# Optimization experiments

Measured on AMD Instinct MI355X. Metric: run time of the kernel, lower is better.

The kernel has to match this reference:

```python
import jax, jax.numpy as jnp
import numpy as np

N = 30000   # nodes
E = 600000  # edges (avg degree 20)
H = 128     # hidden_channels
L = 4       # num_layers
G = 64      # graphs in batch


def _init(key, shape, fan_in):
    return (jax.random.normal(key, shape, jnp.float32) / np.sqrt(fan_in)).astype(jnp.float32)


def setup_inputs() -> dict:
    key = jax.random.key(0)
    ks = jax.random.split(key, 24)
    x = jax.random.normal(ks[0], (N, 1), jnp.float32)
    pos = jax.random.normal(ks[1], (N, 3), jnp.float32)
    edge_index = jax.random.randint(ks[2], (2, E), 0, N, dtype=jnp.int32).astype(jnp.int64)
    batch = jnp.sort(jax.random.randint(ks[3], (N,), 0, G, dtype=jnp.int32)).astype(jnp.int64)

    emb_w = _init(ks[4], (1, H), 1)
    emb_b = jnp.zeros((H,), jnp.float32)

    # stacked per-layer params: msg MLP (2H+1 -> H -> H), node MLP (2H -> H -> H)
    msg_w1 = _init(ks[5], (L, 2 * H + 1, H), 2 * H + 1)
    msg_b1 = jnp.zeros((L, H), jnp.float32)
    msg_w2 = _init(ks[6], (L, H, H), H)
    msg_b2 = jnp.zeros((L, H), jnp.float32)
    node_w1 = _init(ks[7], (L, 2 * H, H), 2 * H)
    node_b1 = jnp.zeros((L, H), jnp.float32)
    node_w2 = _init(ks[8], (L, H, H), H)
    node_b2 = jnp.zeros((L, H), jnp.float32)

    out_w1 = _init(ks[9], (H, 32), H)
    out_b1 = jnp.zeros((32,), jnp.float32)
    out_w2 = _init(ks[10], (32, 1), 32)
    out_b2 = jnp.zeros((1,), jnp.float32)

    return {
        "x": x, "pos": pos, "edge_index": edge_index, "batch": batch,
        "emb_w": emb_w, "emb_b": emb_b,
        "msg_w1": msg_w1, "msg_b1": msg_b1, "msg_w2": msg_w2, "msg_b2": msg_b2,
        "node_w1": node_w1, "node_b1": node_b1, "node_w2": node_w2, "node_b2": node_b2,
        "out_w1": out_w1, "out_b1": out_b1, "out_w2": out_w2, "out_b2": out_b2,
    }


def reference(x, pos, edge_index, batch,
              emb_w, emb_b,
              msg_w1, msg_b1, msg_w2, msg_b2,
              node_w1, node_b1, node_w2, node_b2,
              out_w1, out_b1, out_w2, out_b2):
    row, col = edge_index[0], edge_index[1]  # row = source j, col = target i
    # edge scalar: squared distance (computed once, reused across layers)
    dist_sq = jnp.sum((pos[row] - pos[col]) ** 2, axis=-1, keepdims=True)  # [E,1]

    h = x @ emb_w + emb_b  # [N,H]
    for l in range(L):
        x_j = h[row]   # source features
        x_i = h[col]   # target features
        m = jnp.concatenate([x_i, x_j, dist_sq], axis=-1)           # [E, 2H+1]
        m = jax.nn.silu(m @ msg_w1[l] + msg_b1[l]) @ msg_w2[l] + msg_b2[l]  # [E,H]
        aggr = jax.ops.segment_sum(m, col, num_segments=N)          # scatter-add to targets
        nh = jnp.concatenate([h, aggr], axis=-1)                    # [N, 2H]
        h = jax.nn.silu(nh @ node_w1[l] + node_b1[l]) @ node_w2[l] + node_b2[l]
        # dropout omitted for deterministic reference (eval mode)

    g = jax.ops.segment_sum(h, batch, num_segments=G)               # global_add_pool [G,H]
    return jax.nn.silu(g @ out_w1 + out_b1) @ out_w2 + out_b2       # [G,1]
```

## Files before the change

### kernel.cpp

```cpp
#include <hip/hip_runtime.h>

typedef unsigned short u16;
typedef __bf16 bf16x8 __attribute__((ext_vector_type(8)));
typedef float f32x4 __attribute__((ext_vector_type(4)));

#define HN 128
#define TM 64
#define ASTRIDE 136
#define ECH 256

__device__ __forceinline__ u16 f2bf(float f) {
  union { float f; unsigned u; } v; v.f = f;
  unsigned r = v.u + 0x7fffu + ((v.u >> 16) & 1u);
  return (u16)(r >> 16);
}
__device__ __forceinline__ float bf2f(u16 v) {
  union { unsigned u; float f; } x; x.u = ((unsigned)v) << 16; return x.f;
}
__device__ __forceinline__ float bflo(unsigned v) {
  union { unsigned u; float f; } x; x.u = v << 16; return x.f;
}
__device__ __forceinline__ float bfhi(unsigned v) {
  union { unsigned u; float f; } x; x.u = v & 0xffff0000u; return x.f;
}
__device__ __forceinline__ float silu_f(float x) {
  float e = __builtin_amdgcn_exp2f(-1.442695041f * x);
  return x * __builtin_amdgcn_rcpf(1.f + e);
}

__global__ void pack_weights(const float* __restrict__ msg_w1, const float* __restrict__ msg_w2,
                             const float* __restrict__ node_w1, const float* __restrict__ node_w2,
                             u16* __restrict__ pw, int* __restrict__ deg,
                             float* __restrict__ g, int N_, int GH) {
  int id = blockIdx.x * 256 + threadIdx.x;
  if (id < N_) deg[id] = 0;
  if (id < GH) g[id] = 0.f;
  if (id >= 4 * 6 * 16384) return;
  int l = id / (6 * 16384);
  int rem = id % (6 * 16384);
  int m = rem / 16384;
  int e = rem % 16384;
  int kg = e >> 10;
  int n = (e >> 3) & 127;
  int j = e & 7;
  int k = kg * 8 + j;
  float v = 0.f;
  switch (m) {
    case 0: v = msg_w1[(l * 257 + k) * 128 + n]; break;
    case 1: v = msg_w1[(l * 257 + 128 + k) * 128 + n]; break;
    case 2: v = msg_w2[(l * 128 + k) * 128 + n]; break;
    case 3: v = node_w1[(l * 256 + k) * 128 + n]; break;
    case 4: v = node_w1[(l * 256 + 128 + k) * 128 + n]; break;
    case 5: v = node_w2[(l * 128 + k) * 128 + n]; break;
  }
  pw[id] = f2bf(v);
}

__device__ __forceinline__ void gemm64(const u16* s_A, const u16* s_W,
                                       int w, int quad, int m16, f32x4 acc[8]) {
#pragma unroll
  for (int ks = 0; ks < 4; ks++) {
    bf16x8 a = *(const bf16x8*)&s_A[(w * 16 + m16) * ASTRIDE + ks * 32 + quad * 8];
#pragma unroll
    for (int ct = 0; ct < 8; ct++) {
      bf16x8 b = *(const bf16x8*)&s_W[(ks * 4 + quad) * 1024 + (ct * 16 + m16) * 8];
      acc[ct] = __builtin_amdgcn_mfma_f32_16x16x32_bf16(a, b, acc[ct], 0, 0, 0);
    }
  }
}

__device__ __forceinline__ void gemm64_gb(const u16* s_A, const u16* __restrict__ gW,
                                          int w, int quad, int m16, f32x4 acc[8]) {
#pragma unroll
  for (int ks = 0; ks < 4; ks++) {
    bf16x8 a = *(const bf16x8*)&s_A[(w * 16 + m16) * ASTRIDE + ks * 32 + quad * 8];
#pragma unroll
    for (int ct = 0; ct < 8; ct++) {
      bf16x8 b = *(const bf16x8*)&gW[(ks * 4 + quad) * 1024 + (ct * 16 + m16) * 8];
      acc[ct] = __builtin_amdgcn_mfma_f32_16x16x32_bf16(a, b, acc[ct], 0, 0, 0);
    }
  }
}

__device__ __forceinline__ void gemm64_ra_gb(const bf16x8 aH[4], const u16* __restrict__ gW,
                                             int quad, int m16, f32x4 acc[8]) {
#pragma unroll
  for (int ks = 0; ks < 4; ks++) {
#pragma unroll
    for (int ct = 0; ct < 8; ct++) {
      bf16x8 b = *(const bf16x8*)&gW[(ks * 4 + quad) * 1024 + (ct * 16 + m16) * 8];
      acc[ct] = __builtin_amdgcn_mfma_f32_16x16x32_bf16(aH[ks], b, acc[ct], 0, 0, 0);
    }
  }
}

__global__ __launch_bounds__(256) void fold_kernel(
    const float* __restrict__ msg_w2, const float* __restrict__ node_w1,
    const float* __restrict__ msg_b2, const u16* __restrict__ pw,
    u16* __restrict__ pwc, float* __restrict__ vc) {
  __shared__ __align__(16) u16 s_A[TM * ASTRIDE];
  __shared__ __align__(16) u16 s_W[16384];
  const int t = threadIdx.x;
  const int w = t >> 6, lane = t & 63, quad = lane >> 4, m16 = lane & 15;
  const int b = blockIdx.x, l = b >> 1, half = b & 1;
  const int tile0 = half * 64;

  {
    int r = t >> 2, qo = (t & 3) * 32;
    const float4* src = (const float4*)(msg_w2 + (size_t)(l * 128 + tile0 + r) * 128 + qo);
    u16* dst = s_A + r * ASTRIDE + qo;
#pragma unroll
    for (int i = 0; i < 8; i++) {
      float4 v = src[i];
      ushort4 o;
      o.x = f2bf(v.x); o.y = f2bf(v.y); o.z = f2bf(v.z); o.w = f2bf(v.w);
      *(ushort4*)(dst + i * 4) = o;
    }
  }
  {
    const int4* src = (const int4*)(pw + (size_t)(l * 6 + 4) * 16384);
    int4* dst = (int4*)s_W;
#pragma unroll
    for (int i = 0; i < 8; i++) dst[t + i * 256] = src[t + i * 256];
  }
  __syncthreads();
  f32x4 acc[8];
#pragma unroll
  for (int ct = 0; ct < 8; ct++) acc[ct] = {0.f, 0.f, 0.f, 0.f};
  gemm64(s_A, s_W, w, quad, m16, acc);
#pragma unroll
  for (int ct = 0; ct < 8; ct++)
#pragma unroll
    for (int j = 0; j < 4; j++) {
      int k = tile0 + w * 16 + quad * 4 + j;
      int n = ct * 16 + m16;
      pwc[(size_t)l * 16384 + (k >> 3) * 1024 + n * 8 + (k & 7)] = f2bf(acc[ct][j]);
    }
  if (half == 0 && t < 128) {
    float s = 0.f;
    for (int np = 0; np < 128; np++)
      s += msg_b2[l * 128 + np] * node_w1[(size_t)(l * 256 + 128 + np) * 128 + t];
    vc[l * 128 + t] = s;
  }
}

__global__ void hist_kernel(const int* __restrict__ eidx, int* __restrict__ deg,
                            int* __restrict__ rnk, int E_) {
  int e = blockIdx.x * 256 + threadIdx.x;
  if (e < E_) rnk[e] = atomicAdd(&deg[eidx[E_ + e]], 1);
}

__global__ void scan1_kernel(const int* __restrict__ deg, int* __restrict__ off,
                             int* __restrict__ bsum, int n) {
  __shared__ int s[256];
  int t = threadIdx.x;
  int i = blockIdx.x * 256 + t;
  int v = (i < n) ? deg[i] : 0;
  s[t] = v;
  for (int d = 1; d < 256; d <<= 1) {
    __syncthreads();
    int x = (t >= d) ? s[t - d] : 0;
    __syncthreads();
    s[t] += x;
  }
  __syncthreads();
  if (i < n) off[i] = s[t] - v;
  if (t == 255) bsum[blockIdx.x] = s[255];
}

__global__ void scan2_kernel(int* __restrict__ bsum, int nb) {
  __shared__ int s[256];
  int t = threadIdx.x;
  int v = (t < nb) ? bsum[t] : 0;
  s[t] = v;
  for (int d = 1; d < 256; d <<= 1) {
    __syncthreads();
    int x = (t >= d) ? s[t - d] : 0;
    __syncthreads();
    s[t] += x;
  }
  __syncthreads();
  if (t < nb) bsum[t] = s[t] - v;
}

__global__ void scan3_kernel(int* __restrict__ off, const int* __restrict__ bsum, int n) {
  int i = blockIdx.x * 256 + threadIdx.x;
  if (i < n) off[i] += bsum[blockIdx.x];
}

__global__ void scatter_kernel(const int* __restrict__ eidx, const float* __restrict__ pos,
                               const int* __restrict__ off, const int* __restrict__ rnk,
                               int2* __restrict__ es8, int E_) {
  int e = blockIdx.x * 256 + threadIdx.x;
  if (e >= E_) return;
  int sr = eidx[e], tg = eidx[E_ + e];
  float dx = pos[sr * 3 + 0] - pos[tg * 3 + 0];
  float dy = pos[sr * 3 + 1] - pos[tg * 3 + 1];
  float dz = pos[sr * 3 + 2] - pos[tg * 3 + 2];
  float d = dx * dx + dy * dy + dz * dz;
  int p = off[tg] + rnk[e];
  int2 v;
  v.x = sr | (tg << 15);
  v.y = __float_as_int(d);
  es8[p] = v;
}

__global__ __launch_bounds__(256) void proj_kernel(
    const float* __restrict__ x, const float* __restrict__ emb_w,
    const float* __restrict__ emb_b, u16* __restrict__ hbf,
    u16* __restrict__ Pout, u16* __restrict__ Qout,
    const u16* __restrict__ pw, const float* __restrict__ b1,
    float* __restrict__ S, int NH4, int nblocks, int nnodes) {
  const int t = threadIdx.x;
  const int w = t >> 6, lane = t & 63, quad = lane >> 4, m16 = lane & 15;
  const int tile0 = blockIdx.x * TM;

  {
    float4* S4 = (float4*)S;
    int id = blockIdx.x * 256 + t;
    int stride = nblocks * 256;
    float4 z = {0.f, 0.f, 0.f, 0.f};
    for (int i = id; i < NH4; i += stride) S4[i] = z;
  }

  int nodem = tile0 + w * 16 + m16;
  bool live = nodem < nnodes;
  if (!live) nodem = nnodes - 1;
  float xv = x[nodem];
  bf16x8 aH[4];
#pragma unroll
  for (int ks = 0; ks < 4; ks++) {
    u16 hv[8];
#pragma unroll
    for (int i = 0; i < 8; i++) {
      int c = ks * 32 + quad * 8 + i;
      hv[i] = f2bf(xv * emb_w[c] + emb_b[c]);
    }
    aH[ks] = *(bf16x8*)hv;
    if (live) *(int4*)&hbf[(size_t)nodem * HN + ks * 32 + quad * 8] = *(int4*)hv;
  }
  float bb[8];
#pragma unroll
  for (int ct = 0; ct < 8; ct++) bb[ct] = b1[ct * 16 + m16];

  f32x4 acc[8];
#pragma unroll
  for (int ct = 0; ct < 8; ct++) acc[ct] = {0.f, 0.f, 0.f, 0.f};
  gemm64_ra_gb(aH, pw, quad, m16, acc);
#pragma unroll
  for (int ct = 0; ct < 8; ct++)
#pragma unroll
    for (int j = 0; j < 4; j++) {
      int n = tile0 + w * 16 + quad * 4 + j;
      if (n < nnodes) Pout[(size_t)n * HN + ct * 16 + m16] = f2bf(acc[ct][j] + bb[ct]);
    }
#pragma unroll
  for (int ct = 0; ct < 8; ct++) acc[ct] = {0.f, 0.f, 0.f, 0.f};
  gemm64_ra_gb(aH, pw + 16384, quad, m16, acc);
#pragma unroll
  for (int ct = 0; ct < 8; ct++)
#pragma unroll
    for (int j = 0; j < 4; j++) {
      int n = tile0 + w * 16 + quad * 4 + j;
      if (n < nnodes) Qout[(size_t)n * HN + ct * 16 + m16] = f2bf(acc[ct][j]);
    }
}

__device__ __forceinline__ void edge_step(
    int tg_s, float dd_s, unsigned qv,
    int& cur_s, float& p0, float& p1, float& s0, float& s1,
    const u16* __restrict__ P, float* __restrict__ S, int cp,
    float wd0, float wd1, int tprev_s, int tnext_s) {
  if (tg_s != cur_s) {
    if (cur_s >= 0) {
      float* dst = &S[(size_t)cur_s * HN + cp];
      if (cur_s == tprev_s || cur_s == tnext_s) {
        atomicAdd(dst, s0);
        atomicAdd(dst + 1, s1);
      } else {
        float2 v = {s0, s1};
        *(float2*)dst = v;
      }
    }
    cur_s = tg_s; s0 = 0.f; s1 = 0.f;
    int cg = tg_s < 0 ? 0 : tg_s;
    unsigned pv = *(const unsigned*)&P[(size_t)cg * HN + cp];
    p0 = bflo(pv); p1 = bfhi(pv);
  }
  float x0 = p0 + bflo(qv) + dd_s * wd0;
  float x1 = p1 + bfhi(qv) + dd_s * wd1;
  s0 += silu_f(x0);
  s1 += silu_f(x1);
}

__global__ __launch_bounds__(256) void edge_kernel(
    const u16* __restrict__ P, const u16* __restrict__ Q,
    float* __restrict__ S, const float* __restrict__ w1d,
    const int2* __restrict__ es8, int E_) {
  __shared__ int s_src[ECH + 8];
  __shared__ int s_tgt[ECH + 8];
  __shared__ float s_dist[ECH + 8];

  const int t = threadIdx.x;
  const int e0 = blockIdx.x * ECH;
  {
    int e = e0 + t;
    if (e < E_) {
      int2 v = es8[e];
      s_src[t] = v.x & 0x7fff;
      s_tgt[t] = v.x >> 15;
      s_dist[t] = __int_as_float(v.y);
    } else {
      s_src[t] = 0; s_tgt[t] = -1; s_dist[t] = 0.f;
    }
    if (t < 8) { s_src[ECH + t] = 0; s_tgt[ECH + t] = -1; s_dist[ECH + t] = 0.f; }
  }
  __syncthreads();

  const int lane = t & 63;
  const int w = t >> 6;
  const int cp = lane * 2;
  const int a = w * 64;
  const float2 wdv = *(const float2*)&w1d[cp];
  const float wd0 = wdv.x, wd1 = wdv.y;

  int tprev_s, tnext_s;
  if (w == 0) tprev_s = (e0 > 0) ? (es8[e0 - 1].x >> 15) : -2;
  else tprev_s = s_tgt[a - 1];
  if (w == 3) tnext_s = (e0 + ECH < E_) ? (es8[e0 + ECH].x >> 15) : -2;
  else tnext_s = s_tgt[a + 64];
  tprev_s = __builtin_amdgcn_readfirstlane(tprev_s);
  tnext_s = __builtin_amdgcn_readfirstlane(tnext_s);

  int tg[8];
  float dd[8];
  unsigned qv[8];
#pragma unroll
  for (int j = 0; j < 8; j++) {
    tg[j] = s_tgt[a + j];
    dd[j] = s_dist[a + j];
    qv[j] = *(const unsigned*)&Q[(size_t)s_src[a + j] * HN + cp];
  }

  int cur_s = -1;
  float s0 = 0.f, s1 = 0.f, p0 = 0.f, p1 = 0.f;

#pragma unroll
  for (int i = a; i < a + 64; i += 8) {
    int tgn[8];
    float ddn[8];
    unsigned qvn[8];
#pragma unroll
    for (int j = 0; j < 8; j++) {
      int idx = i + 8 + j;
      tgn[j] = s_tgt[idx];
      ddn[j] = s_dist[idx];
      qvn[j] = *(const unsigned*)&Q[(size_t)s_src[idx] * HN + cp];
    }
#pragma unroll
    for (int j = 0; j < 8; j++) {
      int tg_s = __builtin_amdgcn_readfirstlane(tg[j]);
      edge_step(tg_s, dd[j], qv[j], cur_s, p0, p1, s0, s1, P, S, cp, wd0, wd1, tprev_s, tnext_s);
    }
#pragma unroll
    for (int j = 0; j < 8; j++) { tg[j] = tgn[j]; dd[j] = ddn[j]; qv[j] = qvn[j]; }
  }

  if (cur_s >= 0) {
    float* dst = &S[(size_t)cur_s * HN + cp];
    if (cur_s == tprev_s || cur_s == tnext_s) {
      atomicAdd(dst, s0);
      atomicAdd(dst + 1, s1);
    } else {
      float2 v = {s0, s1};
      *(float2*)dst = v;
    }
  }
}

template <bool FUSE>
__global__ __launch_bounds__(256) void node_kernel(
    const u16* __restrict__ hbf, float* __restrict__ S, const int* __restrict__ deg,
    u16* __restrict__ hout, const u16* __restrict__ pwc, const float* __restrict__ vc,
    const u16* __restrict__ pwn, const float* __restrict__ b1, const float* __restrict__ b2,
    const u16* __restrict__ pw_next, const float* __restrict__ b1_next,
    u16* __restrict__ Pout, u16* __restrict__ Qout, int nnodes) {
  __shared__ __align__(16) u16 s_A[TM * ASTRIDE];
  const int t = threadIdx.x;
  const int w = t >> 6, lane = t & 63, quad = lane >> 4, m16 = lane & 15;
  const int tile0 = blockIdx.x * TM;
  const int rb = lane >> 2;
  const int qo = (lane & 3) * 32;
  u16* band = s_A + (w * 16) * ASTRIDE;

  int node_ = tile0 + w * 16 + rb;
  if (node_ >= nnodes) node_ = nnodes - 1;
  int nodem = tile0 + w * 16 + m16;
  if (nodem >= nnodes) nodem = nnodes - 1;

  float bb1[8], vcr[8], bb2[8], bbn[8];
#pragma unroll
  for (int ct = 0; ct < 8; ct++) {
    bb1[ct] = b1[ct * 16 + m16];
    vcr[ct] = vc[ct * 16 + m16];
    bb2[ct] = b2[ct * 16 + m16];
    bbn[ct] = FUSE ? b1_next[ct * 16 + m16] : 0.f;
  }

  {
    const float4* src = (const float4*)(S + (size_t)node_ * HN + qo);
    u16* dst = band + rb * ASTRIDE + qo;
#pragma unroll
    for (int i = 0; i < 8; i++) {
      float4 v = src[i];
      ushort4 o;
      o.x = f2bf(v.x); o.y = f2bf(v.y); o.z = f2bf(v.z); o.w = f2bf(v.w);
      *(ushort4*)(dst + i * 4) = o;
    }
    float4 z = {0.f, 0.f, 0.f, 0.f};
    float4* zd = (float4*)(S + (size_t)node_ * HN + qo);
#pragma unroll
    for (int i = 0; i < 8; i++) zd[i] = z;
  }
  asm volatile("s_waitcnt lgkmcnt(0)" ::: "memory");
  __builtin_amdgcn_sched_barrier(0);

  f32x4 acc[8];
#pragma unroll
  for (int ct = 0; ct < 8; ct++) acc[ct] = {0.f, 0.f, 0.f, 0.f};
  gemm64_gb(s_A, pwc, w, quad, m16, acc);

  bf16x8 aH[4];
#pragma unroll
  for (int ks = 0; ks < 4; ks++)
    aH[ks] = *(const bf16x8*)&hbf[(size_t)nodem * HN + ks * 32 + quad * 8];
  gemm64_ra_gb(aH, pwn, quad, m16, acc);

  {
    float degv[4];
#pragma unroll
    for (int j = 0; j < 4; j++) {
      int n = tile0 + w * 16 + quad * 4 + j;
      if (n >= nnodes) n = nnodes - 1;
      degv[j] = (float)deg[n];
    }
#pragma unroll
    for (int ct = 0; ct < 8; ct++)
#pragma unroll
      for (int j = 0; j < 4; j++) {
        int row = quad * 4 + j;
        float xv = acc[ct][j] + bb1[ct] + degv[j] * vcr[ct];
        band[row * ASTRIDE + ct * 16 + m16] = f2bf(silu_f(xv));
      }
  }
  asm volatile("s_waitcnt lgkmcnt(0)" ::: "memory");
  __builtin_amdgcn_sched_barrier(0);

#pragma unroll
  for (int ct = 0; ct < 8; ct++) acc[ct] = {0.f, 0.f, 0.f, 0.f};
  gemm64_gb(s_A, pwn + 32768, w, quad, m16, acc);

#pragma unroll
  for (int ct = 0; ct < 8; ct++)
#pragma unroll
    for (int j = 0; j < 4; j++) {
      int row = quad * 4 + j;
      int n = tile0 + w * 16 + row;
      u16 hv = f2bf(acc[ct][j] + bb2[ct]);
      if (n < nnodes) hout[(size_t)n * HN + ct * 16 + m16] = hv;
      if (FUSE) band[row * ASTRIDE + ct * 16 + m16] = hv;
    }

  if (FUSE) {
    asm volatile("s_waitcnt lgkmcnt(0)" ::: "memory");
    __builtin_amdgcn_sched_barrier(0);
#pragma unroll
    for (int ct = 0; ct < 8; ct++) acc[ct] = {0.f, 0.f, 0.f, 0.f};
    gemm64_gb(s_A, pw_next, w, quad, m16, acc);
#pragma unroll
    for (int ct = 0; ct < 8; ct++)
#pragma unroll
      for (int j = 0; j < 4; j++) {
        int n = tile0 + w * 16 + quad * 4 + j;
        if (n < nnodes) Pout[(size_t)n * HN + ct * 16 + m16] = f2bf(acc[ct][j] + bbn[ct]);
      }
#pragma unroll
    for (int ct = 0; ct < 8; ct++) acc[ct] = {0.f, 0.f, 0.f, 0.f};
    gemm64_gb(s_A, pw_next + 16384, w, quad, m16, acc);
#pragma unroll
    for (int ct = 0; ct < 8; ct++)
#pragma unroll
      for (int j = 0; j < 4; j++) {
        int n = tile0 + w * 16 + quad * 4 + j;
        if (n < nnodes) Qout[(size_t)n * HN + ct * 16 + m16] = f2bf(acc[ct][j]);
      }
  }
}

__global__ __launch_bounds__(256) void pool_kernel(
    const u16* __restrict__ h, const int* __restrict__ batch,
    float* __restrict__ g, int N) {
  __shared__ int s_b[64];
  const int t = threadIdx.x;
  const int n0 = blockIdx.x * 64;
  if (t < 64) {
    int n = n0 + t;
    s_b[t] = (n < N) ? batch[n] : -1;
  }
  __syncthreads();
  const int cp = (t & 63) * 2;
  const int rg = t >> 6;
  int cur = -1;
  float s0 = 0.f, s1 = 0.f;
#pragma unroll 4
  for (int i = 0; i < 16; i++) {
    int r = rg * 16 + i;
    int b = s_b[r];
    if (b < 0) break;
    if (b != cur) {
      if (cur >= 0) {
        atomicAdd(&g[cur * HN + cp], s0);
        atomicAdd(&g[cur * HN + cp + 1], s1);
      }
      cur = b; s0 = 0.f; s1 = 0.f;
    }
    unsigned v = *(const unsigned*)&h[(size_t)(n0 + r) * HN + cp];
    s0 += bf2f((u16)(v & 0xffffu));
    s1 += bf2f((u16)(v >> 16));
  }
  if (cur >= 0) {
    atomicAdd(&g[cur * HN + cp], s0);
    atomicAdd(&g[cur * HN + cp + 1], s1);
  }
}

__global__ __launch_bounds__(64) void out_kernel(
    const float* __restrict__ g, const float* __restrict__ w1,
    const float* __restrict__ b1, const float* __restrict__ w2,
    const float* __restrict__ b2, float* __restrict__ out) {
  const int gi = blockIdx.x;
  const int t = threadIdx.x;
  const int c = t & 31, kh = t >> 5;
  float s = 0.f;
  for (int k = kh * 64; k < kh * 64 + 64; k++)
    s += g[gi * HN + k] * w1[k * 32 + c];
  s += __shfl_down(s, 32);
  float r = 0.f;
  if (kh == 0) r = silu_f(s + b1[c]) * w2[c];
  r += __shfl_down(r, 16);
  r += __shfl_down(r, 8);
  r += __shfl_down(r, 4);
  r += __shfl_down(r, 2);
  r += __shfl_down(r, 1);
  if (t == 0) out[gi] = r + b2[0];
}

extern "C" void kernel_launch(void* const* d_in, const int* in_sizes, int n_in,
                              void* d_out, int out_size, void* d_ws, size_t ws_size,
                              hipStream_t stream) {
  const float* x = (const float*)d_in[0];
  const float* pos = (const float*)d_in[1];
  const int* eidx = (const int*)d_in[2];
  const int* batch = (const int*)d_in[3];
  const float* emb_w = (const float*)d_in[4];
  const float* emb_b = (const float*)d_in[5];
  const float* msg_w1 = (const float*)d_in[6];
  const float* msg_b1 = (const float*)d_in[7];
  const float* msg_w2 = (const float*)d_in[8];
  const float* msg_b2 = (const float*)d_in[9];
  const float* node_w1 = (const float*)d_in[10];
  const float* node_b1 = (const float*)d_in[11];
  const float* node_w2 = (const float*)d_in[12];
  const float* node_b2 = (const float*)d_in[13];
  const float* out_w1 = (const float*)d_in[14];
  const float* out_b1 = (const float*)d_in[15];
  const float* out_w2 = (const float*)d_in[16];
  const float* out_b2 = (const float*)d_in[17];
  float* outp = (float*)d_out;

  const int N = 30000, E = 600000, G = 64;
  const size_t NH = (size_t)N * HN;

  u16* hA = (u16*)d_ws;
  u16* hB = hA + NH;
  u16* Pp = hB + NH;
  u16* Qp = Pp + NH;
  float* S = (float*)(Qp + NH);
  int2* es8 = (int2*)(S + NH);
  int* deg = (int*)(es8 + E);
  int* off = deg + N;
  int* bsum = off + N;
  float* g = (float*)(bsum + 128);
  u16* pw = (u16*)(g + G * HN);
  u16* pwc = pw + (size_t)4 * 6 * 16384;
  float* vcb = (float*)(pwc + (size_t)4 * 16384);
  int* rnk = (int*)S;

  const int NB = (N + 255) / 256;
  const int NTB = (N + TM - 1) / TM;

  pack_weights<<<(4 * 6 * 16384 + 255) / 256, 256, 0, stream>>>(
      msg_w1, msg_w2, node_w1, node_w2, pw, deg, g, N, G * HN);
  fold_kernel<<<8, 256, 0, stream>>>(msg_w2, node_w1, msg_b2, pw, pwc, vcb);

  hist_kernel<<<(E + 255) / 256, 256, 0, stream>>>(eidx, deg, rnk, E);
  scan1_kernel<<<NB, 256, 0, stream>>>(deg, off, bsum, N);
  scan2_kernel<<<1, 256, 0, stream>>>(bsum, NB);
  scan3_kernel<<<NB, 256, 0, stream>>>(off, bsum, N);
  scatter_kernel<<<(E + 255) / 256, 256, 0, stream>>>(eidx, pos, off, rnk, es8, E);

  proj_kernel<<<NTB, 256, 0, stream>>>(x, emb_w, emb_b, hA, Pp, Qp, pw, msg_b1,
                                       S, (int)(NH / 4), NTB, N);

  u16* hcur = hA;
  u16* hnext = hB;
  for (int l = 0; l < 4; l++) {
    const u16* pwl = pw + (size_t)(l * 6) * 16384;
    edge_kernel<<<(E + ECH - 1) / ECH, 256, 0, stream>>>(
        Pp, Qp, S,
        msg_w1 + (size_t)(l * 257 + 256) * 128,
        es8, E);
    if (l < 3) {
      const u16* pw_next = pw + (size_t)((l + 1) * 6) * 16384;
      node_kernel<true><<<NTB, 256, 0, stream>>>(
          hcur, S, deg, hnext, pwc + (size_t)l * 16384, vcb + l * 128,
          pwl + 3 * 16384, node_b1 + l * 128, node_b2 + l * 128,
          pw_next, msg_b1 + (l + 1) * 128, Pp, Qp, N);
    } else {
      node_kernel<false><<<NTB, 256, 0, stream>>>(
          hcur, S, deg, hnext, pwc + (size_t)l * 16384, vcb + l * 128,
          pwl + 3 * 16384, node_b1 + l * 128, node_b2 + l * 128,
          nullptr, nullptr, nullptr, nullptr, N);
    }
    u16* tmp = hcur; hcur = hnext; hnext = tmp;
  }

  pool_kernel<<<(N + 63) / 64, 256, 0, stream>>>(hcur, batch, g, N);
  out_kernel<<<G, 64, 0, stream>>>(g, out_w1, out_b1, out_w2, out_b2, outp);
}
```

Measured before the change: 413.5 us.

## Fuse edge aggregation into per-tile node kernel with LDS accumulation

Merges the edge kernel into the node kernel: each 64-node block walks its CSR-sorted edge range and accumulates messages into a shared-memory tile. This removes the global S buffer, its zeroing and global atomics, and one launch per layer, and P/Q are double-buffered so the next layer's projections do not overwrite inputs still being read. The cost is 32KB extra LDS per block, which lowers occupancy, and per-block edge work that varies with node degree, with only 4 waves per block doing the gather.

```diff
diff --git a/kernel.cpp b/kernel.cpp
--- a/kernel.cpp
+++ b/kernel.cpp
@@ -7,7 +7,6 @@
 #define HN 128
 #define TM 64
 #define ASTRIDE 136
-#define ECH 256
 
 __device__ __forceinline__ u16 f2bf(float f) {
   union { float f; unsigned u; } v; v.f = f;
@@ -209,19 +208,10 @@
     const float* __restrict__ x, const float* __restrict__ emb_w,
     const float* __restrict__ emb_b, u16* __restrict__ hbf,
     u16* __restrict__ Pout, u16* __restrict__ Qout,
-    const u16* __restrict__ pw, const float* __restrict__ b1,
-    float* __restrict__ S, int NH4, int nblocks, int nnodes) {
+    const u16* __restrict__ pw, const float* __restrict__ b1, int nnodes) {
   const int t = threadIdx.x;
   const int w = t >> 6, lane = t & 63, quad = lane >> 4, m16 = lane & 15;
   const int tile0 = blockIdx.x * TM;
-
-  {
-    float4* S4 = (float4*)S;
-    int id = blockIdx.x * 256 + t;
-    int stride = nblocks * 256;
-    float4 z = {0.f, 0.f, 0.f, 0.f};
-    for (int i = id; i < NH4; i += stride) S4[i] = z;
-  }
 
   int nodem = tile0 + w * 16 + m16;
   bool live = nodem < nnodes;
@@ -266,21 +256,16 @@
     }
 }
 
-__device__ __forceinline__ void edge_step(
+__device__ __forceinline__ void edge_step_lds(
     int tg_s, float dd_s, unsigned qv,
     int& cur_s, float& p0, float& p1, float& s0, float& s1,
-    const u16* __restrict__ P, float* __restrict__ S, int cp,
-    float wd0, float wd1, int tprev_s, int tnext_s) {
+    const u16* __restrict__ P, float* s_S, int cp,
+    float wd0, float wd1, int tile0) {
   if (tg_s != cur_s) {
     if (cur_s >= 0) {
-      float* dst = &S[(size_t)cur_s * HN + cp];
-      if (cur_s == tprev_s || cur_s == tnext_s) {
-        atomicAdd(dst, s0);
-        atomicAdd(dst + 1, s1);
-      } else {
-        float2 v = {s0, s1};
-        *(float2*)dst = v;
-      }
+      float* dst = &s_S[(cur_s - tile0) * HN + cp];
+      atomicAdd(dst, s0);
+      atomicAdd(dst + 1, s1);
     }
     cur_s = tg_s; s0 = 0.f; s1 = 0.f;
     int cg = tg_s < 0 ? 0 : tg_s;
@@ -293,108 +278,117 @@
   s1 += silu_f(x1);
 }
 
-__global__ __launch_bounds__(256) void edge_kernel(
+template <bool FUSE>
+__global__ __launch_bounds__(256) void layer_kernel(
     const u16* __restrict__ P, const u16* __restrict__ Q,
-    float* __restrict__ S, const float* __restrict__ w1d,
-    const int2* __restrict__ es8, int E_) {
-  __shared__ int s_src[ECH + 8];
-  __shared__ int s_tgt[ECH + 8];
-  __shared__ float s_dist[ECH + 8];
-
-  const int t = threadIdx.x;
-  const int e0 = blockIdx.x * ECH;
-  {
-    int e = e0 + t;
-    if (e < E_) {
-      int2 v = es8[e];
-      s_src[t] = v.x & 0x7fff;
-      s_tgt[t] = v.x >> 15;
-      s_dist[t] = __int_as_float(v.y);
-    } else {
-      s_src[t] = 0; s_tgt[t] = -1; s_dist[t] = 0.f;
-    }
-    if (t < 8) { s_src[ECH + t] = 0; s_tgt[ECH + t] = -1; s_dist[ECH + t] = 0.f; }
-  }
-  __syncthreads();
-
-  const int lane = t & 63;
-  const int w = t >> 6;
-  const int cp = lane * 2;
-  const int a = w * 64;
-  const float2 wdv = *(const float2*)&w1d[cp];
-  const float wd0 = wdv.x, wd1 = wdv.y;
-
-  int tprev_s, tnext_s;
-  if (w == 0) tprev_s = (e0 > 0) ? (es8[e0 - 1].x >> 15) : -2;
-  else tprev_s = s_tgt[a - 1];
-  if (w == 3) tnext_s = (e0 + ECH < E_) ? (es8[e0 + ECH].x >> 15) : -2;
-  else tnext_s = s_tgt[a + 64];
-  tprev_s = __builtin_amdgcn_readfirstlane(tprev_s);
-  tnext_s = __builtin_amdgcn_readfirstlane(tnext_s);
-
-  int tg[8];
-  float dd[8];
-  unsigned qv[8];
-#pragma unroll
-  for (int j = 0; j < 8; j++) {
-    tg[j] = s_tgt[a + j];
-    dd[j] = s_dist[a + j];
-    qv[j] = *(const unsigned*)&Q[(size_t)s_src[a + j] * HN + cp];
-  }
-
-  int cur_s = -1;
-  float s0 = 0.f, s1 = 0.f, p0 = 0.f, p1 = 0.f;
-
-#pragma unroll
-  for (int i = a; i < a + 64; i += 8) {
-    int tgn[8];
-    float ddn[8];
-    unsigned qvn[8];
-#pragma unroll
-    for (int j = 0; j < 8; j++) {
-      int idx = i + 8 + j;
-      tgn[j] = s_tgt[idx];
-      ddn[j] = s_dist[idx];
-      qvn[j] = *(const unsigned*)&Q[(size_t)s_src[idx] * HN + cp];
-    }
-#pragma unroll
-    for (int j = 0; j < 8; j++) {
-      int tg_s = __builtin_amdgcn_readfirstlane(tg[j]);
-      edge_step(tg_s, dd[j], qv[j], cur_s, p0, p1, s0, s1, P, S, cp, wd0, wd1, tprev_s, tnext_s);
-    }
-#pragma unroll
-    for (int j = 0; j < 8; j++) { tg[j] = tgn[j]; dd[j] = ddn[j]; qv[j] = qvn[j]; }
-  }
-
-  if (cur_s >= 0) {
-    float* dst = &S[(size_t)cur_s * HN + cp];
-    if (cur_s == tprev_s || cur_s == tnext_s) {
-      atomicAdd(dst, s0);
-      atomicAdd(dst + 1, s1);
-    } else {
-      float2 v = {s0, s1};
-      *(float2*)dst = v;
-    }
-  }
-}
-
-template <bool FUSE>
-__global__ __launch_bounds__(256) void node_kernel(
-    const u16* __restrict__ hbf, float* __restrict__ S, const int* __restrict__ deg,
-    u16* __restrict__ hout, const u16* __restrict__ pwc, const float* __restrict__ vc,
+    const u16* __restrict__ hbf, u16* __restrict__ hout,
+    const int* __restrict__ off, const int* __restrict__ deg,
+    const float* __restrict__ w1d, const int2* __restrict__ es8,
+    const u16* __restrict__ pwc, const float* __restrict__ vc,
     const u16* __restrict__ pwn, const float* __restrict__ b1, const float* __restrict__ b2,
     const u16* __restrict__ pw_next, const float* __restrict__ b1_next,
-    u16* __restrict__ Pout, u16* __restrict__ Qout, int nnodes) {
+    u16* __restrict__ Pout, u16* __restrict__ Qout, int nnodes, int E_) {
+  __shared__ float s_S[TM * HN];
   __shared__ __align__(16) u16 s_A[TM * ASTRIDE];
   const int t = threadIdx.x;
   const int w = t >> 6, lane = t & 63, quad = lane >> 4, m16 = lane & 15;
   const int tile0 = blockIdx.x * TM;
+  u16* band = s_A + (w * 16) * ASTRIDE;
+
+  {
+    float4 z = {0.f, 0.f, 0.f, 0.f};
+    float4* p4 = (float4*)s_S;
+#pragma unroll
+    for (int i = 0; i < 8; i++) p4[t + i * 256] = z;
+  }
+  __syncthreads();
+
+  const int cp = lane * 2;
+  const float2 wdv = *(const float2*)&w1d[cp];
+  const float wd0 = wdv.x, wd1 = wdv.y;
+  const int e_lo = off[tile0];
+  const int e_hi = (tile0 + TM < nnodes) ? off[tile0 + TM] : E_;
+  const int span = e_hi - e_lo;
+  const int wstart = e_lo + (span * w) / 4;
+  const int wend = e_lo + (span * (w + 1)) / 4;
+  const int total = wend - wstart;
+  const int nchunks = (total + 63) >> 6;
+
+  int cur_s = -1;
+  float s0 = 0.f, s1 = 0.f, p0 = 0.f, p1 = 0.f;
+
+  if (nchunks > 0) {
+    int2* ebuf = (int2*)band;
+    {
+      int e = wstart + lane;
+      int2 v;
+      if (e < wend) v = es8[e];
+      else { v.x = (int)0xFFFF8000; v.y = 0; }
+      ebuf[lane] = v;
+    }
+    asm volatile("s_waitcnt lgkmcnt(0)" ::: "memory");
+    int tg[8]; float dd[8]; unsigned qv[8];
+#pragma unroll
+    for (int j = 0; j < 8; j++) {
+      int2 v = ebuf[j];
+      tg[j] = v.x >> 15; dd[j] = __int_as_float(v.y);
+      qv[j] = *(const unsigned*)&Q[(size_t)(v.x & 0x7fff) * HN + cp];
+    }
+
+    for (int ci = 0; ci < nchunks; ci++) {
+      const int2* cb = ebuf + (ci & 1) * 64;
+      const int2* nb = ebuf + ((ci + 1) & 1) * 64;
+      int2 vnext; vnext.x = (int)0xFFFF8000; vnext.y = 0;
+      {
+        int e = wstart + (ci + 1) * 64 + lane;
+        if (ci + 1 < nchunks && e < wend) vnext = es8[e];
+      }
+#pragma unroll
+      for (int g = 0; g < 7; g++) {
+        int tgn[8]; float ddn[8]; unsigned qvn[8];
+#pragma unroll
+        for (int j = 0; j < 8; j++) {
+          int2 v = cb[(g + 1) * 8 + j];
+          tgn[j] = v.x >> 15; ddn[j] = __int_as_float(v.y);
+          qvn[j] = *(const unsigned*)&Q[(size_t)(v.x & 0x7fff) * HN + cp];
+        }
+#pragma unroll
+        for (int j = 0; j < 8; j++) {
+          int tg_s = __builtin_amdgcn_readfirstlane(tg[j]);
+          edge_step_lds(tg_s, dd[j], qv[j], cur_s, p0, p1, s0, s1, P, s_S, cp, wd0, wd1, tile0);
+        }
+#pragma unroll
+        for (int j = 0; j < 8; j++) { tg[j] = tgn[j]; dd[j] = ddn[j]; qv[j] = qvn[j]; }
+      }
+      ebuf[((ci + 1) & 1) * 64 + lane] = vnext;
+      asm volatile("s_waitcnt lgkmcnt(0)" ::: "memory");
+      {
+        int tgn[8]; float ddn[8]; unsigned qvn[8];
+#pragma unroll
+        for (int j = 0; j < 8; j++) {
+          int2 v = nb[j];
+          tgn[j] = v.x >> 15; ddn[j] = __int_as_float(v.y);
+          qvn[j] = *(const unsigned*)&Q[(size_t)(v.x & 0x7fff) * HN + cp];
+        }
+#pragma unroll
+        for (int j = 0; j < 8; j++) {
+          int tg_s = __builtin_amdgcn_readfirstlane(tg[j]);
+          edge_step_lds(tg_s, dd[j], qv[j], cur_s, p0, p1, s0, s1, P, s_S, cp, wd0, wd1, tile0);
+        }
+#pragma unroll
+        for (int j = 0; j < 8; j++) { tg[j] = tgn[j]; dd[j] = ddn[j]; qv[j] = qvn[j]; }
+      }
+    }
+    if (cur_s >= 0) {
+      float* dst = &s_S[(cur_s - tile0) * HN + cp];
+      atomicAdd(dst, s0);
+      atomicAdd(dst + 1, s1);
+    }
+  }
+  __syncthreads();
+
   const int rb = lane >> 2;
   const int qo = (lane & 3) * 32;
-  u16* band = s_A + (w * 16) * ASTRIDE;
-
-  int node_ = tile0 + w * 16 + rb;
-  if (node_ >= nnodes) node_ = nnodes - 1;
   int nodem = tile0 + w * 16 + m16;
   if (nodem >= nnodes) nodem = nnodes - 1;
 
@@ -408,7 +402,7 @@
   }
 
   {
-    const float4* src = (const float4*)(S + (size_t)node_ * HN + qo);
+    const float4* src = (const float4*)&s_S[(w * 16 + rb) * HN + qo];
     u16* dst = band + rb * ASTRIDE + qo;
 #pragma unroll
     for (int i = 0; i < 8; i++) {
@@ -417,10 +411,6 @@
       o.x = f2bf(v.x); o.y = f2bf(v.y); o.z = f2bf(v.z); o.w = f2bf(v.w);
       *(ushort4*)(dst + i * 4) = o;
     }
-    float4 z = {0.f, 0.f, 0.f, 0.f};
-    float4* zd = (float4*)(S + (size_t)node_ * HN + qo);
-#pragma unroll
-    for (int i = 0; i < 8; i++) zd[i] = z;
   }
   asm volatile("s_waitcnt lgkmcnt(0)" ::: "memory");
   __builtin_amdgcn_sched_barrier(0);
@@ -583,10 +573,11 @@
 
   u16* hA = (u16*)d_ws;
   u16* hB = hA + NH;
-  u16* Pp = hB + NH;
-  u16* Qp = Pp + NH;
-  float* S = (float*)(Qp + NH);
-  int2* es8 = (int2*)(S + NH);
+  u16* Pa = hB + NH;
+  u16* Qa = Pa + NH;
+  u16* Pb = Qa + NH;
+  u16* Qb = Pb + NH;
+  int2* es8 = (int2*)(Qb + NH);
   int* deg = (int*)(es8 + E);
   int* off = deg + N;
   int* bsum = off + N;
@@ -594,7 +585,7 @@
   u16* pw = (u16*)(g + G * HN);
   u16* pwc = pw + (size_t)4 * 6 * 16384;
   float* vcb = (float*)(pwc + (size_t)4 * 16384);
-  int* rnk = (int*)S;
+  int* rnk = (int*)Pb;
 
   const int NB = (N + 255) / 256;
   const int NTB = (N + TM - 1) / TM;
@@ -609,30 +600,32 @@
   scan3_kernel<<<NB, 256, 0, stream>>>(off, bsum, N);
   scatter_kernel<<<(E + 255) / 256, 256, 0, stream>>>(eidx, pos, off, rnk, es8, E);
 
-  proj_kernel<<<NTB, 256, 0, stream>>>(x, emb_w, emb_b, hA, Pp, Qp, pw, msg_b1,
-                                       S, (int)(NH / 4), NTB, N);
+  proj_kernel<<<NTB, 256, 0, stream>>>(x, emb_w, emb_b, hA, Pa, Qa, pw, msg_b1, N);
 
   u16* hcur = hA;
   u16* hnext = hB;
+  u16* Pin = Pa; u16* Qin = Qa;
+  u16* Pot = Pb; u16* Qot = Qb;
   for (int l = 0; l < 4; l++) {
     const u16* pwl = pw + (size_t)(l * 6) * 16384;
-    edge_kernel<<<(E + ECH - 1) / ECH, 256, 0, stream>>>(
-        Pp, Qp, S,
-        msg_w1 + (size_t)(l * 257 + 256) * 128,
-        es8, E);
+    const float* w1d = msg_w1 + (size_t)(l * 257 + 256) * 128;
     if (l < 3) {
       const u16* pw_next = pw + (size_t)((l + 1) * 6) * 16384;
-      node_kernel<true><<<NTB, 256, 0, stream>>>(
-          hcur, S, deg, hnext, pwc + (size_t)l * 16384, vcb + l * 128,
+      layer_kernel<true><<<NTB, 256, 0, stream>>>(
+          Pin, Qin, hcur, hnext, off, deg, w1d, es8,
+          pwc + (size_t)l * 16384, vcb + l * 128,
           pwl + 3 * 16384, node_b1 + l * 128, node_b2 + l * 128,
-          pw_next, msg_b1 + (l + 1) * 128, Pp, Qp, N);
+          pw_next, msg_b1 + (l + 1) * 128, Pot, Qot, N, E);
     } else {
-      node_kernel<false><<<NTB, 256, 0, stream>>>(
-          hcur, S, deg, hnext, pwc + (size_t)l * 16384, vcb + l * 128,
+      layer_kernel<false><<<NTB, 256, 0, stream>>>(
+          Pin, Qin, hcur, hnext, off, deg, w1d, es8,
+          pwc + (size_t)l * 16384, vcb + l * 128,
           pwl + 3 * 16384, node_b1 + l * 128, node_b2 + l * 128,
-          nullptr, nullptr, nullptr, nullptr, N);
+          nullptr, nullptr, nullptr, nullptr, N, E);
     }
     u16* tmp = hcur; hcur = hnext; hnext = tmp;
+    tmp = Pin; Pin = Pot; Pot = tmp;
+    tmp = Qin; Qin = Qot; Qot = tmp;
   }
 
   pool_kernel<<<(N + 63) / 64, 256, 0, stream>>>(hcur, batch, g, N);
```

Result: slower. 435.2 us (+5.2%).
